# Performance work log

Measured on AMD Instinct MI355X. Metric: run time of the kernel, lower is better.

Reference implementation:

```python
import jax, jax.numpy as jnp
import numpy as np

B, H, W = 2, 512, 512


def _conv(x, w, b):
    y = jax.lax.conv_general_dilated(
        x, w, window_strides=(1, 1), padding='SAME',
        dimension_numbers=('NCHW', 'OIHW', 'NCHW'))
    return y + b[None, :, None, None]


def _pool(x):
    return jax.lax.reduce_window(x, -jnp.inf, jax.lax.max,
                                 (1, 1, 2, 2), (1, 1, 2, 2), 'VALID')


def _vgg_pools(x, ws, bs):
    # vgg16.features up to modules 4, 9, 16 (the first three maxpools)
    r = jax.nn.relu
    x = r(_conv(x, ws[0], bs[0]))
    x = r(_conv(x, ws[1], bs[1]))
    p1 = _pool(x)                      # [B,64,256,256]  (module 4)
    x = r(_conv(p1, ws[2], bs[2]))
    x = r(_conv(x, ws[3], bs[3]))
    p2 = _pool(x)                      # [B,128,128,128] (module 9)
    x = r(_conv(p2, ws[4], bs[4]))
    x = r(_conv(x, ws[5], bs[5]))
    x = r(_conv(x, ws[6], bs[6]))
    p3 = _pool(x)                      # [B,256,64,64]   (module 16)
    return (p1, p2, p3)


def _style(a, g):
    # faithful to per-(b,c) torch.mm(phi.T, phi): WxW Gram per channel
    Bc, C, Hc, Wc = a.shape
    Kp = 1.0 / (C * Hc * Wc)
    Ga = jnp.einsum('bchw,bchv->bcwv', a, a)
    Gg = jnp.einsum('bchw,bchv->bcwv', g, g)
    return jnp.sum(jnp.abs(Kp * (Ga - Gg))) / (C * C)


def setup_inputs() -> dict:
    key = jax.random.key(0)
    ks = jax.random.split(key, 20)
    igt = jax.random.normal(ks[0], (B, 3, H, W), dtype=jnp.float32)
    iout = jax.random.normal(ks[1], (B, 3, H, W), dtype=jnp.float32)
    mask = jax.random.randint(ks[2], (B, 1, H, W), 0, 2).astype(jnp.float32)
    # VGG16 conv stack up to features[16]: channel plan per torchvision vgg16
    chans = [(3, 64), (64, 64), (64, 128), (128, 128), (128, 256), (256, 256), (256, 256)]
    inp = {'igt': igt, 'iout': iout, 'mask': mask}
    for i, (cin, cout) in enumerate(chans):
        scale = np.sqrt(2.0 / (cin * 9)).astype(np.float32)
        inp[f'w{i}'] = jax.random.normal(ks[3 + i], (cout, cin, 3, 3), dtype=jnp.float32) * scale
        inp[f'b{i}'] = jnp.zeros((cout,), dtype=jnp.float32)
    return inp


def reference(igt, iout, mask, w0, b0, w1, b1, w2, b2, w3, b3, w4, b4, w5, b5, w6, b6):
    ws = (w0, w1, w2, w3, w4, w5, w6)
    bs = (b0, b1, b2, b3, b4, b5, b6)
    m = jnp.where(mask != 0, 1.0, 0.0).astype(igt.dtype)   # mask[mask!=0]=1
    icomp = jnp.where(m == 1, igt, iout)                   # make_comp (broadcast over C)
    Bn = igt.shape[0]
    N = 3 * H * W * Bn
    diff = iout - igt
    # l_hole: original loops B times over the FULL norm -> factor B (faithful)
    l_hole = Bn * jnp.sum(jnp.abs((1.0 - m) * diff)) / N
    # l_valid: per-sample norms summed == full L1
    l_valid = jnp.sum(jnp.abs(m * diff)) / N
    pool_out = _vgg_pools(iout, ws, bs)
    pool_gt = _vgg_pools(igt, ws, bs)
    pool_comp = _vgg_pools(icomp, ws, bs)
    # l_perc: original always normalizes by prod(pool_gt[0].shape) (faithful bug)
    Nigt = float(np.prod(pool_gt[0].shape))
    l_perc = 0.0
    for i in range(3):
        l_perc = l_perc + (jnp.sum(jnp.abs(pool_out[i] - pool_gt[i]))
                           + jnp.sum(jnp.abs(pool_comp[i] - pool_gt[i]))) / Nigt
    l_style_comp = sum(_style(pool_comp[i], pool_gt[i]) for i in range(3))
    l_style_out = sum(_style(pool_out[i], pool_gt[i]) for i in range(3))
    return l_hole + l_valid + l_perc + l_style_comp + l_style_out
```

## Files before the change

kernel.cpp:

```cpp
#include <hip/hip_runtime.h>
#include <hip/hip_bf16.h>


typedef __attribute__((ext_vector_type(8))) short bf16x8_t;
typedef __attribute__((ext_vector_type(4))) float f32x4_t;
typedef __attribute__((ext_vector_type(16))) float f32x16_t;
typedef __attribute__((ext_vector_type(8))) int i32x8_t;

typedef const __attribute__((address_space(1))) void* gas_t;
typedef __attribute__((address_space(3))) void* las_t;

__device__ __forceinline__ void gld16(const void* g, void* l) {
  __builtin_amdgcn_global_load_lds((gas_t)g, (las_t)l, 16, 0, 0);
}

__device__ __forceinline__ unsigned char f2fp8(float v) {
  return (unsigned char)(__builtin_amdgcn_cvt_pk_fp8_f32(v, v, 0, false) & 0xff);
}

__device__ __forceinline__ i32x8_t ld_frag(const unsigned char* lds, int row,
                                           int h) {
  const int sw = (row >> 1) & 3;
  const unsigned char* base = lds + row * 64;
  uint4 lo = *(const uint4*)(base + (((2 * h) ^ sw) << 4));
  uint4 hi = *(const uint4*)(base + (((2 * h + 1) ^ sw) << 4));
  i32x8_t r;
  r[0] = lo.x; r[1] = lo.y; r[2] = lo.z; r[3] = lo.w;
  r[4] = hi.x; r[5] = hi.y; r[6] = hi.z; r[7] = hi.w;
  return r;
}

__device__ __forceinline__ i32x8_t ld32g(const unsigned char* p) {
  uint4 lo = *(const uint4*)p;
  uint4 hi = *(const uint4*)(p + 16);
  i32x8_t r;
  r[0] = lo.x; r[1] = lo.y; r[2] = lo.z; r[3] = lo.w;
  r[4] = hi.x; r[5] = hi.y; r[6] = hi.z; r[7] = hi.w;
  return r;
}

__device__ __forceinline__ float blk_sum256(float v, float* s4) {
#pragma unroll
  for (int o = 32; o > 0; o >>= 1) v += __shfl_down(v, o);
  int w = threadIdx.x >> 6;
  if ((threadIdx.x & 63) == 0) s4[w] = v;
  __syncthreads();
  float r = s4[0] + s4[1] + s4[2] + s4[3];
  __syncthreads();
  return r;
}

__global__ void init_slots(float* slots) {
  if (threadIdx.x < 32) slots[threadIdx.x] = 0.0f;
}

__global__ __launch_bounds__(256) void l1_kernel(
    const float* __restrict__ igt, const float* __restrict__ iout,
    const float* __restrict__ mask, float* __restrict__ slots) {
  __shared__ float s4[4];
  float ah = 0.0f, av = 0.0f;
  for (int idx = blockIdx.x * 256 + threadIdx.x; idx < 1572864;
       idx += gridDim.x * 256) {
    int pix = idx & 262143;
    int n = idx / 786432;
    float mk = mask[n * 262144 + pix];
    bool m = (mk != 0.0f);
    float d = fabsf(iout[idx] - igt[idx]);
    if (m) av += d; else ah += d;
  }
  float r = blk_sum256(ah, s4);
  if (threadIdx.x == 0) atomicAdd(&slots[0], r);
  r = blk_sum256(av, s4);
  if (threadIdx.x == 0) atomicAdd(&slots[1], r);
}

__global__ __launch_bounds__(256) void pack_w(const float* __restrict__ w,
                                              unsigned char* __restrict__ wp,
                                              int Cin, int Cout) {
  int i = blockIdx.x * 256 + threadIdx.x;
  int c4n = Cin >> 2;
  if (i >= Cout * c4n * 9) return;
  int o = i % 9;
  int rem = i / 9;
  int c4 = rem % c4n;
  int co = rem / c4n;
  int dy = o / 3, dx = o % 3;
  unsigned r = 0;
#pragma unroll
  for (int k = 0; k < 4; ++k) {
    int ci = c4 * 4 + k;
    float v = w[((co * Cin + ci) * 3 + dy) * 3 + dx];
    r |= (unsigned)f2fp8(v) << (8 * k);
  }
  *(unsigned*)(wp + ((long)(o * Cout + co)) * Cin + c4 * 4) = r;
}

__global__ __launch_bounds__(256) void pack_w1(const float* __restrict__ w,
                                               __hip_bfloat16* __restrict__ wk) {
  int i = blockIdx.x * 256 + threadIdx.x;
  if (i >= 64 * 32) return;
  int co = i >> 5, k = i & 31;
  float v = 0.0f;
  if (k < 27) {
    int dy = k / 9, r = k - dy * 9;
    int dx = r / 3, ci = r - dx * 3;
    v = w[((co * 3 + ci) * 3 + dy) * 3 + dx];
  }
  wk[i] = __float2bfloat16(v);
}

__global__ __launch_bounds__(256) void pack2_kernel(
    const float* __restrict__ igt, const float* __restrict__ iout,
    const float* __restrict__ mask, __hip_bfloat16* __restrict__ apk, int sid,
    int n0, int NB) {
  int idx = blockIdx.x * 256 + threadIdx.x;
  if (idx >= NB * 262144) return;
  int nl = idx >> 18;
  int pix = idx & 262143;
  int y = pix >> 9, x = pix & 511;
  int sample = n0 + nl;
  __align__(16) __hip_bfloat16 buf[32];
#pragma unroll
  for (int k = 27; k < 32; ++k) buf[k] = __float2bfloat16(0.0f);
  for (int dy = 0; dy < 3; ++dy)
    for (int dx = 0; dx < 3; ++dx) {
      int gy = y - 1 + dy, gx = x - 1 + dx;
      bool inb = (gy >= 0 && gy < 512 && gx >= 0 && gx < 512);
      int p = gy * 512 + gx;
      bool useG;
      if (sid == 0) useG = true;
      else if (sid == 1) useG = false;
      else useG = inb && (mask[sample * 262144 + (inb ? p : 0)] != 0.0f);
      const float* src = useG ? igt : iout;
#pragma unroll
      for (int ci = 0; ci < 3; ++ci) {
        float v = inb ? src[sample * 786432 + ci * 262144 + p] : 0.0f;
        buf[dy * 9 + dx * 3 + ci] = __float2bfloat16(v);
      }
    }
  __hip_bfloat16* dst = apk + (long)idx * 32;
#pragma unroll
  for (int q = 0; q < 4; ++q)
    *(uint4*)&dst[q * 8] = *(const uint4*)&buf[q * 8];
}

__global__ __launch_bounds__(256, 2) void conv1m(
    const __hip_bfloat16* __restrict__ apk, const __hip_bfloat16* __restrict__ wk,
    const float* __restrict__ bias, unsigned char* __restrict__ out) {
  __shared__ __align__(16) short ApS[512 * 32];
  __shared__ __align__(16) short BwS[64 * 32];
  const int tid = threadIdx.x;
  const int lane = tid & 63;
  const int wv = tid >> 6;
  const int quad = lane >> 4, l15 = lane & 15;
  const int n = blockIdx.z;
  const int x0 = blockIdx.x << 6;
  const int y0 = blockIdx.y << 3;
  const int spos = lane >> 2;
  const int sq = lane & 3;

  for (int u = wv; u < 32; u += 4) {
    int pos = (u << 4) + spos;
    int r = pos >> 6, c = pos & 63;
    gld16(apk + (((long)n * 512 + y0 + r) * 512 + x0 + c) * 32 + sq * 8,
          &ApS[u << 9]);
  }
  if (wv < 4) gld16(wk + spos * 32 + sq * 8, &BwS[wv << 9]);
  __syncthreads();

  f32x4_t acc[8][4];
#pragma unroll
  for (int mt = 0; mt < 8; ++mt)
#pragma unroll
    for (int nt = 0; nt < 4; ++nt) acc[mt][nt] = (f32x4_t)0.0f;

  bf16x8_t bf[4];
#pragma unroll
  for (int nt = 0; nt < 4; ++nt)
    bf[nt] = *(const bf16x8_t*)&BwS[(nt * 16 + l15) * 32 + quad * 8];
#pragma unroll
  for (int mt = 0; mt < 8; ++mt) {
    const int rl = 2 * wv + (mt >> 2);
    const int pl = (mt & 3) * 16 + l15;
    const bf16x8_t a = *(const bf16x8_t*)&ApS[(rl * 64 + pl) * 32 + quad * 8];
#pragma unroll
    for (int nt = 0; nt < 4; ++nt)
      acc[mt][nt] = __builtin_amdgcn_mfma_f32_16x16x32_bf16(a, bf[nt],
                                                            acc[mt][nt], 0, 0, 0);
  }

  float bv[4];
#pragma unroll
  for (int nt = 0; nt < 4; ++nt) bv[nt] = bias[nt * 16 + l15];

  __syncthreads();
  unsigned char* O8 = (unsigned char*)ApS;
#pragma unroll
  for (int mt = 0; mt < 8; ++mt) {
    const int ry = 2 * wv + (mt >> 2);
#pragma unroll
    for (int nt = 0; nt < 4; ++nt) {
      const int col = nt * 16 + l15;
#pragma unroll
      for (int reg = 0; reg < 4; ++reg) {
        int px = (mt & 3) * 16 + quad * 4 + reg;
        float v = fmaxf(acc[mt][nt][reg] + bv[nt], 0.0f);
        O8[((ry << 6) + px) * 64 + col] = f2fp8(v);
      }
    }
  }
  __syncthreads();
#pragma unroll
  for (int j = 0; j < 8; ++j) {
    int L = (j * 256 + tid) << 4;
    int x = (L >> 6) & 63;
    int cq = L & 63;
    *(uint4*)(out + (((long)n * 512 + y0 + j) * 512 + x0 + x) * 64 + cq) =
        *(const uint4*)&O8[L];
  }
}

__global__ __launch_bounds__(256, 3) void conv_f8(
    const unsigned char* __restrict__ act, const unsigned char* __restrict__ wp,
    const float* __restrict__ bias, unsigned char* __restrict__ out,
    const unsigned char* __restrict__ zp, int Cin, int Cout, int H, int W) {
  __shared__ __align__(16) unsigned char ApS[400 * 64];
  const int tid = threadIdx.x;
  const int lane = tid & 63;
  const int wv = tid >> 6;
  const int l31 = lane & 31;
  const int h = lane >> 5;
  const int pr = wv & 1;
  const int ch = wv >> 1;
  const int coB = Cout >> 6;
  const int n = blockIdx.z / coB;
  const int co0 = (blockIdx.z % coB) << 6;
  const int x0 = blockIdx.x << 6;
  const int y0 = blockIdx.y << 2;
  const int spos = lane >> 2;
  const int sc = lane & 3;

  f32x16_t acc[2][2];
#pragma unroll
  for (int dr = 0; dr < 2; ++dr)
#pragma unroll
    for (int mh = 0; mh < 2; ++mh) acc[dr][mh] = (f32x16_t)0.0f;

  for (int cb = 0; cb < Cin; cb += 64) {
    if (cb) __syncthreads();
    for (int u = wv; u < 25; u += 4) {
      int pos = (u << 4) + spos;
      int q = sc ^ ((pos >> 1) & 3);
      int r = pos / 66, c = pos - r * 66;
      int gy = y0 - 1 + r, gx = x0 - 1 + c;
      const unsigned char* src = zp;
      if (pos < 396 && gy >= 0 && gy < H && gx >= 0 && gx < W)
        src = act + ((long)((long)n * H + gy) * W + gx) * Cin + cb + (q << 4);
      gld16(src, &ApS[u << 10]);
    }
    __syncthreads();

    const unsigned char* wl =
        wp + ((long)(co0 + (ch << 5) + l31)) * Cin + cb + (h << 5);
#pragma unroll
    for (int dx = 0; dx < 3; ++dx) {
      i32x8_t Af[2][4];
#pragma unroll
      for (int mh = 0; mh < 2; ++mh)
#pragma unroll
        for (int ri = 0; ri < 4; ++ri)
          Af[mh][ri] =
              ld_frag(ApS, (2 * pr + ri) * 66 + mh * 32 + l31 + dx, h);
#pragma unroll
      for (int dy = 0; dy < 3; ++dy) {
        const int o = dy * 3 + dx;
        i32x8_t Bf = ld32g(wl + (long)o * Cout * Cin);
#pragma unroll
        for (int dr = 0; dr < 2; ++dr)
#pragma unroll
          for (int mh = 0; mh < 2; ++mh)
            acc[dr][mh] = __builtin_amdgcn_mfma_scale_f32_32x32x64_f8f6f4(
                Af[mh][dr + dy], Bf, acc[dr][mh], 0, 0, 0,
                0x7F7F7F7F, 0, 0x7F7F7F7F);
      }
    }
  }

  const float bv = bias[co0 + (ch << 5) + l31];

  __syncthreads();
#pragma unroll
  for (int dr = 0; dr < 2; ++dr) {
    const int ry = 2 * pr + dr;
#pragma unroll
    for (int mh = 0; mh < 2; ++mh) {
#pragma unroll
      for (int reg = 0; reg < 16; ++reg) {
        int rowM = (reg & 3) + 8 * (reg >> 2) + 4 * h;
        int x = mh * 32 + rowM;
        float v = fmaxf(acc[dr][mh][reg] + bv, 0.0f);
        ApS[((ry << 6) + x) * 64 + (ch << 5) + l31] = f2fp8(v);
      }
    }
  }
  __syncthreads();
#pragma unroll
  for (int j = 0; j < 4; ++j) {
    int L = (j * 256 + tid) << 4;
    int ry = L >> 12;
    int x = (L >> 6) & 63;
    int cq = L & 63;
    *(uint4*)(out + (((long)n * H + y0 + ry) * W + x0 + x) * Cout + co0 + cq) =
        *(const uint4*)&ApS[L];
  }
}

__global__ __launch_bounds__(256, 3) void conv_f8p(
    const unsigned char* __restrict__ act, const unsigned char* __restrict__ wp,
    const float* __restrict__ bias, unsigned char* __restrict__ outF,
    __hip_bfloat16* __restrict__ outB, const unsigned char* __restrict__ zp,
    int Cin, int Cout, int H, int W) {
  __shared__ __align__(16) unsigned char ApS[400 * 64];
  const int tid = threadIdx.x;
  const int lane = tid & 63;
  const int wv = tid >> 6;
  const int l31 = lane & 31;
  const int h = lane >> 5;
  const int pr = wv & 1;
  const int ch = wv >> 1;
  const int coB = Cout >> 6;
  const int n = blockIdx.z / coB;
  const int co0 = (blockIdx.z % coB) << 6;
  const int x0g = blockIdx.x << 6;
  const int y0 = blockIdx.y << 2;
  const int spos = lane >> 2;
  const int sc = lane & 3;

  f32x16_t acc[2][2];
#pragma unroll
  for (int dr = 0; dr < 2; ++dr)
#pragma unroll
    for (int mh = 0; mh < 2; ++mh) acc[dr][mh] = (f32x16_t)0.0f;

  for (int cb = 0; cb < Cin; cb += 64) {
    if (cb) __syncthreads();
    for (int u = wv; u < 25; u += 4) {
      int pos = (u << 4) + spos;
      int q = sc ^ ((pos >> 1) & 3);
      int r = pos / 66, c = pos - r * 66;
      int gy = y0 - 1 + r, gx = x0g - 1 + c;
      const unsigned char* src = zp;
      if (pos < 396 && gy >= 0 && gy < H && gx >= 0 && gx < W)
        src = act + ((long)((long)n * H + gy) * W + gx) * Cin + cb + (q << 4);
      gld16(src, &ApS[u << 10]);
    }
    __syncthreads();

    const unsigned char* wl =
        wp + ((long)(co0 + (ch << 5) + l31)) * Cin + cb + (h << 5);
#pragma unroll
    for (int dx = 0; dx < 3; ++dx) {
      i32x8_t Af[2][4];
#pragma unroll
      for (int mh = 0; mh < 2; ++mh)
#pragma unroll
        for (int ri = 0; ri < 4; ++ri)
          Af[mh][ri] =
              ld_frag(ApS, (2 * pr + ri) * 66 + mh * 32 + l31 + dx, h);
#pragma unroll
      for (int dy = 0; dy < 3; ++dy) {
        const int o = dy * 3 + dx;
        i32x8_t Bf = ld32g(wl + (long)o * Cout * Cin);
#pragma unroll
        for (int dr = 0; dr < 2; ++dr)
#pragma unroll
          for (int mh = 0; mh < 2; ++mh)
            acc[dr][mh] = __builtin_amdgcn_mfma_scale_f32_32x32x64_f8f6f4(
                Af[mh][dr + dy], Bf, acc[dr][mh], 0, 0, 0,
                0x7F7F7F7F, 0, 0x7F7F7F7F);
      }
    }
  }

  const int Ho = H >> 1, Wo = W >> 1;
  const int ho0 = blockIdx.y << 1;
  const int wo0 = blockIdx.x << 5;
  const float bv = bias[co0 + (ch << 5) + l31];

  __syncthreads();
  unsigned char* F8 = ApS;
  __hip_bfloat16* BB = (__hip_bfloat16*)(ApS + 4096);
#pragma unroll
  for (int mh = 0; mh < 2; ++mh) {
#pragma unroll
    for (int p8 = 0; p8 < 8; ++p8) {
      const int reg = 2 * p8;
      float m0 = fmaxf(fmaxf(acc[0][mh][reg], acc[0][mh][reg + 1]),
                       fmaxf(acc[1][mh][reg], acc[1][mh][reg + 1]));
      float v = fmaxf(m0 + bv, 0.0f);
      int rowM = (reg & 3) + 8 * (reg >> 2) + 4 * h;
      int wo = mh * 16 + (rowM >> 1);
      int off = ((pr * 32 + wo) << 6) + (ch << 5) + l31;
      F8[off] = f2fp8(v);
      BB[off] = __float2bfloat16(v);
    }
  }
  __syncthreads();
  {
    int L = tid << 4;
    int hl = L >> 11;
    int wo = (L >> 6) & 31;
    int cq = L & 63;
    *(uint4*)(outF + (((long)n * Ho + ho0 + hl) * Wo + wo0 + wo) * Cout + co0 +
              cq) = *(const uint4*)&F8[L];
  }
#pragma unroll
  for (int j = 0; j < 2; ++j) {
    int S = (j * 256 + tid) << 3;
    int hl = S >> 11;
    int wo = (S >> 6) & 31;
    int cq = S & 63;
    *(uint4*)(outB + (((long)n * Ho + ho0 + hl) * Wo + wo0 + wo) * Cout + co0 +
              cq) = *(const uint4*)&BB[S];
  }
}

__global__ __launch_bounds__(256) void transpose_k(
    const __hip_bfloat16* __restrict__ in, __hip_bfloat16* __restrict__ out,
    int C, int Ho, int Wo) {
  const int cl = threadIdx.x & 31;
  const int wl = threadIdx.x >> 5;
  const int cg = C >> 5;
  const int j = blockIdx.z / cg;
  const int c = (blockIdx.z % cg) * 32 + cl;
  const int wo = blockIdx.x * 8 + wl;
  const int ho0 = blockIdx.y * 8;
  __align__(16) __hip_bfloat16 res[8];
#pragma unroll
  for (int i = 0; i < 8; ++i)
    res[i] = in[(((long)j * Ho + ho0 + i) * Wo + wo) * C + c];
  *(uint4*)&out[((long)(j * C + c) * Wo + wo) * Ho + ho0] =
      *(const uint4*)res;
}

__global__ __launch_bounds__(256) void perc_kernel(
    const __hip_bfloat16* __restrict__ gt, const __hip_bfloat16* __restrict__ cur,
    int M8, float* __restrict__ slots) {
  __shared__ float s4[4];
  const uint4* g4 = (const uint4*)gt;
  const uint4* c4 = (const uint4*)cur;
  float acc = 0.0f;
  for (int i = blockIdx.x * 256 + threadIdx.x; i < M8; i += gridDim.x * 256) {
    uint4 g = g4[i], c = c4[i];
    const unsigned* gu = (const unsigned*)&g;
    const unsigned* cu = (const unsigned*)&c;
#pragma unroll
    for (int k = 0; k < 4; ++k) {
      float g0 = __uint_as_float(gu[k] << 16);
      float g1 = __uint_as_float(gu[k] & 0xffff0000u);
      float c0 = __uint_as_float(cu[k] << 16);
      float c1 = __uint_as_float(cu[k] & 0xffff0000u);
      acc += fabsf(c0 - g0) + fabsf(c1 - g1);
    }
  }
  float r = blk_sum256(acc, s4);
  if (threadIdx.x == 0) atomicAdd(&slots[2], r);
}

template <int BM>
__global__ __launch_bounds__(256) void gram_mfma(
    const __hip_bfloat16* __restrict__ gt_p,
    const __hip_bfloat16* __restrict__ cur_p, int Wp, int Hp, float fscale,
    float* __restrict__ slots) {
  constexpr int COLS = BM + 64;
  constexpr int WR = BM / 4;
  constexpr int MT = WR / 16;
  __shared__ __align__(16) short S[2 * COLS * 40];
  __shared__ float s4[4];
  const int tid = threadIdx.x;
  const int lane = tid & 63;
  const int wvi = tid >> 6;
  const int quad = lane >> 4, l15 = lane & 15;
  const int vt = blockIdx.x * 64;
  const int wt = blockIdx.y * BM;
  const long plane = (long)blockIdx.z * Wp * Hp;
  const __hip_bfloat16* bases[2] = {gt_p + plane, cur_p + plane};

  f32x4_t acc[2][MT][4];
#pragma unroll
  for (int t = 0; t < 2; ++t)
#pragma unroll
    for (int mt = 0; mt < MT; ++mt)
#pragma unroll
      for (int nt = 0; nt < 4; ++nt) acc[t][mt][nt] = (f32x4_t)0.0f;

  const int nchunk = 2 * COLS * 4;
  for (int h0 = 0; h0 < Hp; h0 += 32) {
    for (int e = tid; e < nchunk; e += 256) {
      int chunk = e & 3;
      int colt = e >> 2;
      int t = colt / COLS;
      int col = colt - t * COLS;
      int sc = (col < BM) ? (wt + col) : (vt + col - BM);
      uint4 v = *(const uint4*)(bases[t] + (long)sc * Hp + h0 + chunk * 8);
      *(uint4*)&S[(t * COLS + col) * 40 + chunk * 8] = v;
    }
    __syncthreads();
#pragma unroll
    for (int t = 0; t < 2; ++t) {
      bf16x8_t bf[4];
#pragma unroll
      for (int nt = 0; nt < 4; ++nt)
        bf[nt] = *(const bf16x8_t*)&S[(t * COLS + BM + nt * 16 + l15) * 40 +
                                      quad * 8];
#pragma unroll
      for (int mt = 0; mt < MT; ++mt) {
        bf16x8_t a = *(const bf16x8_t*)&S[(t * COLS + wvi * WR + mt * 16 + l15) *
                                              40 + quad * 8];
#pragma unroll
        for (int nt = 0; nt < 4; ++nt)
          acc[t][mt][nt] = __builtin_amdgcn_mfma_f32_16x16x32_bf16(
              a, bf[nt], acc[t][mt][nt], 0, 0, 0);
      }
    }
    __syncthreads();
  }

  float local = 0.0f;
#pragma unroll
  for (int mt = 0; mt < MT; ++mt)
#pragma unroll
    for (int nt = 0; nt < 4; ++nt)
#pragma unroll
      for (int reg = 0; reg < 4; ++reg)
        local += fabsf(acc[1][mt][nt][reg] - acc[0][mt][nt][reg]);
  float r = blk_sum256(local, s4);
  if (tid == 0) atomicAdd(&slots[3], r * fscale);
}

__global__ void combine_kernel(const float* __restrict__ slots,
                               float* __restrict__ out) {
  if (threadIdx.x == 0) {
    const float Nn = 1572864.0f;
    const float Nigt = 8388608.0f;
    out[0] = 2.0f * slots[0] / Nn + slots[1] / Nn + slots[2] / Nigt + slots[3];
  }
}

extern "C" void kernel_launch(void* const* d_in, const int* in_sizes, int n_in,
                              void* d_out, int out_size, void* d_ws,
                              size_t ws_size, hipStream_t stream) {
  (void)in_sizes; (void)n_in; (void)out_size;
  const float* igt = (const float*)d_in[0];
  const float* iout = (const float*)d_in[1];
  const float* mask = (const float*)d_in[2];
  const float* w[7];
  const float* b[7];
  for (int i = 0; i < 7; ++i) {
    w[i] = (const float*)d_in[3 + 2 * i];
    b[i] = (const float*)d_in[4 + 2 * i];
  }
  float* slots = (float*)d_ws;
  const unsigned char* zp = (const unsigned char*)d_ws + 64;

  unsigned char* wpk = (unsigned char*)((char*)d_ws + 256);
  const long wpOff[6] = {0, 36864, 110592, 258048, 552960, 1142784};
  const int wpCin[6] = {64, 64, 128, 128, 256, 256};
  const int wpCout[6] = {64, 128, 128, 256, 256, 256};
  __hip_bfloat16* w1k = (__hip_bfloat16*)((char*)d_ws + 256 + 1732608);

  const size_t NEED2 = 194674944ULL;
  const int NB = (ws_size >= NEED2) ? 2 : 1;
  const int B3 = 3 * NB;

  char* base = (char*)d_ws + 1736960;
  __hip_bfloat16* Apk = (__hip_bfloat16*)base;
  unsigned char* Y1 = (unsigned char*)(base + (size_t)NB * 16777216);
  unsigned char* P1N8 = (unsigned char*)(base + (size_t)NB * 33554432);
  __hip_bfloat16* P1Nb = (__hip_bfloat16*)(base + (size_t)NB * 46137344);
  __hip_bfloat16* pgT1 = (__hip_bfloat16*)(base + (size_t)NB * 54525952);
  __hip_bfloat16* pcT1 = (__hip_bfloat16*)(base + (size_t)NB * 62914560);
  __hip_bfloat16* P2Nb = (__hip_bfloat16*)(base + (size_t)NB * 71303168);
  __hip_bfloat16* P2T = (__hip_bfloat16*)(base + (size_t)NB * 83886080);
  unsigned char* T = (unsigned char*)base;
  unsigned char* P2N8 = (unsigned char*)(base + (size_t)NB * 46137344);
  unsigned char* Y5 = (unsigned char*)base;
  unsigned char* Y6 = (unsigned char*)(base + (size_t)NB * 12582912);
  __hip_bfloat16* P3Nb = (__hip_bfloat16*)(base + (size_t)NB * 33554432);
  __hip_bfloat16* P3T = (__hip_bfloat16*)(base + (size_t)NB * 39845888);
  unsigned char* P3N8 = (unsigned char*)(base + (size_t)NB * 46137344);

  const float fs1 = (float)(1.0 / (4194304.0 * 4096.0));
  const float fs2 = (float)(1.0 / (2097152.0 * 16384.0));
  const float fs3 = (float)(1.0 / (1048576.0 * 65536.0));

  init_slots<<<1, 64, 0, stream>>>(slots);
  l1_kernel<<<304, 256, 0, stream>>>(igt, iout, mask, slots);
  for (int l = 0; l < 6; ++l) {
    int elems = wpCout[l] * (wpCin[l] >> 2) * 9;
    pack_w<<<(elems + 255) / 256, 256, 0, stream>>>(w[l + 1], wpk + wpOff[l],
                                                    wpCin[l], wpCout[l]);
  }
  pack_w1<<<8, 256, 0, stream>>>(w[0], w1k);

  for (int n0 = 0; n0 < 2; n0 += NB) {
    for (int s = 0; s < 3; ++s) {
      pack2_kernel<<<NB * 1024, 256, 0, stream>>>(igt, iout, mask, Apk, s, n0, NB);
      conv1m<<<dim3(8, 64, NB), 256, 0, stream>>>(Apk, w1k, b[0], Y1);
      conv_f8p<<<dim3(8, 128, NB), 256, 0, stream>>>(
          Y1, wpk + wpOff[0], b[1], P1N8 + (size_t)s * NB * 4194304, P1Nb, zp,
          64, 64, 512, 512);
      transpose_k<<<dim3(32, 32, NB * 2), 256, 0, stream>>>(
          P1Nb, (s ? pcT1 : pgT1), 64, 256, 256);
      if (s > 0) {
        perc_kernel<<<304, 256, 0, stream>>>(pgT1, pcT1, NB * 524288, slots);
        gram_mfma<128><<<dim3(4, 2, NB * 64), 256, 0, stream>>>(
            pgT1, pcT1, 256, 256, fs1, slots);
      }
    }
    conv_f8<<<dim3(4, 64, B3 * 2), 256, 0, stream>>>(
        P1N8, wpk + wpOff[1], b[2], T, zp, 64, 128, 256, 256);
    conv_f8p<<<dim3(4, 64, B3 * 2), 256, 0, stream>>>(
        T, wpk + wpOff[2], b[3], P2N8, P2Nb, zp, 128, 128, 256, 256);
    transpose_k<<<dim3(16, 16, B3 * 4), 256, 0, stream>>>(P2Nb, P2T, 128, 128, 128);
    for (int s = 1; s <= 2; ++s) {
      perc_kernel<<<304, 256, 0, stream>>>(
          P2T, P2T + (size_t)s * NB * 2097152, NB * 262144, slots);
      gram_mfma<128><<<dim3(2, 1, NB * 128), 256, 0, stream>>>(
          P2T, P2T + (size_t)s * NB * 2097152, 128, 128, fs2, slots);
    }
    conv_f8<<<dim3(2, 32, B3 * 4), 256, 0, stream>>>(
        P2N8, wpk + wpOff[3], b[4], Y5, zp, 128, 256, 128, 128);
    conv_f8<<<dim3(2, 32, B3 * 4), 256, 0, stream>>>(
        Y5, wpk + wpOff[4], b[5], Y6, zp, 256, 256, 128, 128);
    conv_f8p<<<dim3(2, 32, B3 * 4), 256, 0, stream>>>(
        Y6, wpk + wpOff[5], b[6], P3N8, P3Nb, zp, 256, 256, 128, 128);
    transpose_k<<<dim3(8, 8, B3 * 8), 256, 0, stream>>>(P3Nb, P3T, 256, 64, 64);
    for (int s = 1; s <= 2; ++s) {
      perc_kernel<<<304, 256, 0, stream>>>(
          P3T, P3T + (size_t)s * NB * 1048576, NB * 131072, slots);
      gram_mfma<64><<<dim3(1, 1, NB * 256), 256, 0, stream>>>(
          P3T, P3T + (size_t)s * NB * 1048576, 64, 64, fs3, slots);
    }
  }

  combine_kernel<<<1, 64, 0, stream>>>(slots, (float*)d_out);
}
```

Measured before the change: 828.4 us.

## Double-buffer LDS staging in fp8 convs and process two row tiles per block

```diff
diff --git a/kernel.cpp b/kernel.cpp
--- a/kernel.cpp
+++ b/kernel.cpp
@@ -220,11 +220,11 @@
   }
 }
 
-__global__ __launch_bounds__(256, 3) void conv_f8(
+__global__ __launch_bounds__(256, 2) void conv_f8(
     const unsigned char* __restrict__ act, const unsigned char* __restrict__ wp,
     const float* __restrict__ bias, unsigned char* __restrict__ out,
     const unsigned char* __restrict__ zp, int Cin, int Cout, int H, int W) {
-  __shared__ __align__(16) unsigned char ApS[400 * 64];
+  __shared__ __align__(16) unsigned char ApS[2][28 * 1024];
   const int tid = threadIdx.x;
   const int lane = tid & 63;
   const int wv = tid >> 6;
@@ -236,32 +236,60 @@
   const int n = blockIdx.z / coB;
   const int co0 = (blockIdx.z % coB) << 6;
   const int x0 = blockIdx.x << 6;
-  const int y0 = blockIdx.y << 2;
+  const int y0base = blockIdx.y << 3;
   const int spos = lane >> 2;
   const int sc = lane & 3;
-
-  f32x16_t acc[2][2];
-#pragma unroll
-  for (int dr = 0; dr < 2; ++dr)
-#pragma unroll
-    for (int mh = 0; mh < 2; ++mh) acc[dr][mh] = (f32x16_t)0.0f;
-
-  for (int cb = 0; cb < Cin; cb += 64) {
-    if (cb) __syncthreads();
-    for (int u = wv; u < 25; u += 4) {
-      int pos = (u << 4) + spos;
+  const int CB = Cin >> 6;
+  const int NU = 2 * CB;
+  const float bv = bias[co0 + (ch << 5) + l31];
+
+  auto STAGE = [&](int u) {
+    const int t = u / CB;
+    const int cb64 = (u - t * CB) << 6;
+    const int ty0 = y0base + t * 4;
+    unsigned char* dst = ApS[u & 1];
+    for (int uu = wv; uu < 28; uu += 4) {
+      int pos = (uu << 4) + spos;
       int q = sc ^ ((pos >> 1) & 3);
       int r = pos / 66, c = pos - r * 66;
-      int gy = y0 - 1 + r, gx = x0 - 1 + c;
+      int gy = ty0 - 1 + r, gx = x0 - 1 + c;
       const unsigned char* src = zp;
       if (pos < 396 && gy >= 0 && gy < H && gx >= 0 && gx < W)
-        src = act + ((long)((long)n * H + gy) * W + gx) * Cin + cb + (q << 4);
-      gld16(src, &ApS[u << 10]);
-    }
-    __syncthreads();
+        src = act + ((long)((long)n * H + gy) * W + gx) * Cin + cb64 + (q << 4);
+      gld16(src, dst + (uu << 10));
+    }
+  };
+
+  f32x16_t acc[2][2];
+#pragma unroll
+  for (int dr = 0; dr < 2; ++dr)
+#pragma unroll
+    for (int mh = 0; mh < 2; ++mh) acc[dr][mh] = (f32x16_t)0.0f;
+
+  STAGE(0);
+  for (int u = 0; u < NU; ++u) {
+    const int t = u / CB;
+    const int cb = u - t * CB;
+    const int ty0 = y0base + t * 4;
+    if (u == 0) {
+      asm volatile("s_waitcnt vmcnt(0)" ::: "memory");
+    } else if (cb == 0) {
+      asm volatile("s_waitcnt vmcnt(4)" ::: "memory");
+    } else {
+      asm volatile("s_waitcnt vmcnt(0)" ::: "memory");
+    }
+    __builtin_amdgcn_s_barrier();
 
     const unsigned char* wl =
-        wp + ((long)(co0 + (ch << 5) + l31)) * Cin + cb + (h << 5);
+        wp + ((long)(co0 + (ch << 5) + l31)) * Cin + (cb << 6) + (h << 5);
+    i32x8_t Bh[9];
+#pragma unroll
+    for (int o = 0; o < 9; ++o) Bh[o] = ld32g(wl + (long)o * Cout * Cin);
+    __builtin_amdgcn_sched_barrier(0);
+    if (u + 1 < NU) STAGE(u + 1);
+    __builtin_amdgcn_sched_barrier(0);
+
+    const unsigned char* A = ApS[u & 1];
 #pragma unroll
     for (int dx = 0; dx < 3; ++dx) {
       i32x8_t Af[2][4];
@@ -269,58 +297,61 @@
       for (int mh = 0; mh < 2; ++mh)
 #pragma unroll
         for (int ri = 0; ri < 4; ++ri)
-          Af[mh][ri] =
-              ld_frag(ApS, (2 * pr + ri) * 66 + mh * 32 + l31 + dx, h);
+          Af[mh][ri] = ld_frag(A, (2 * pr + ri) * 66 + mh * 32 + l31 + dx, h);
 #pragma unroll
       for (int dy = 0; dy < 3; ++dy) {
-        const int o = dy * 3 + dx;
-        i32x8_t Bf = ld32g(wl + (long)o * Cout * Cin);
 #pragma unroll
         for (int dr = 0; dr < 2; ++dr)
 #pragma unroll
           for (int mh = 0; mh < 2; ++mh)
             acc[dr][mh] = __builtin_amdgcn_mfma_scale_f32_32x32x64_f8f6f4(
-                Af[mh][dr + dy], Bf, acc[dr][mh], 0, 0, 0,
+                Af[mh][dr + dy], Bh[dy * 3 + dx], acc[dr][mh], 0, 0, 0,
                 0x7F7F7F7F, 0, 0x7F7F7F7F);
       }
     }
-  }
-
-  const float bv = bias[co0 + (ch << 5) + l31];
-
-  __syncthreads();
-#pragma unroll
-  for (int dr = 0; dr < 2; ++dr) {
-    const int ry = 2 * pr + dr;
-#pragma unroll
-    for (int mh = 0; mh < 2; ++mh) {
-#pragma unroll
-      for (int reg = 0; reg < 16; ++reg) {
-        int rowM = (reg & 3) + 8 * (reg >> 2) + 4 * h;
-        int x = mh * 32 + rowM;
-        float v = fmaxf(acc[dr][mh][reg] + bv, 0.0f);
-        ApS[((ry << 6) + x) * 64 + (ch << 5) + l31] = f2fp8(v);
-      }
-    }
-  }
-  __syncthreads();
-#pragma unroll
-  for (int j = 0; j < 4; ++j) {
-    int L = (j * 256 + tid) << 4;
-    int ry = L >> 12;
-    int x = (L >> 6) & 63;
-    int cq = L & 63;
-    *(uint4*)(out + (((long)n * H + y0 + ry) * W + x0 + x) * Cout + co0 + cq) =
-        *(const uint4*)&ApS[L];
-  }
-}
-
-__global__ __launch_bounds__(256, 3) void conv_f8p(
+
+    if (cb == CB - 1) {
+      unsigned char* O8 = ApS[u & 1];
+      __builtin_amdgcn_s_barrier();
+#pragma unroll
+      for (int dr = 0; dr < 2; ++dr) {
+        const int ry = 2 * pr + dr;
+#pragma unroll
+        for (int mh = 0; mh < 2; ++mh) {
+#pragma unroll
+          for (int reg = 0; reg < 16; ++reg) {
+            int rowM = (reg & 3) + 8 * (reg >> 2) + 4 * h;
+            int x = mh * 32 + rowM;
+            float v = fmaxf(acc[dr][mh][reg] + bv, 0.0f);
+            O8[((ry << 6) + x) * 64 + (ch << 5) + l31] = f2fp8(v);
+          }
+        }
+      }
+      asm volatile("s_waitcnt lgkmcnt(0)" ::: "memory");
+      __builtin_amdgcn_s_barrier();
+#pragma unroll
+      for (int j = 0; j < 4; ++j) {
+        int L = (j * 256 + tid) << 4;
+        int ry = L >> 12;
+        int x = (L >> 6) & 63;
+        int cq = L & 63;
+        *(uint4*)(out + (((long)n * H + ty0 + ry) * W + x0 + x) * Cout + co0 +
+                  cq) = *(const uint4*)&O8[L];
+      }
+#pragma unroll
+      for (int dr = 0; dr < 2; ++dr)
+#pragma unroll
+        for (int mh = 0; mh < 2; ++mh) acc[dr][mh] = (f32x16_t)0.0f;
+    }
+  }
+}
+
+__global__ __launch_bounds__(256, 2) void conv_f8p(
     const unsigned char* __restrict__ act, const unsigned char* __restrict__ wp,
     const float* __restrict__ bias, unsigned char* __restrict__ outF,
     __hip_bfloat16* __restrict__ outB, const unsigned char* __restrict__ zp,
     int Cin, int Cout, int H, int W) {
-  __shared__ __align__(16) unsigned char ApS[400 * 64];
+  __shared__ __align__(16) unsigned char ApS[2][28 * 1024];
   const int tid = threadIdx.x;
   const int lane = tid & 63;
   const int wv = tid >> 6;
@@ -331,33 +362,63 @@
   const int coB = Cout >> 6;
   const int n = blockIdx.z / coB;
   const int co0 = (blockIdx.z % coB) << 6;
-  const int x0g = blockIdx.x << 6;
-  const int y0 = blockIdx.y << 2;
+  const int x0 = blockIdx.x << 6;
+  const int y0base = blockIdx.y << 3;
   const int spos = lane >> 2;
   const int sc = lane & 3;
-
-  f32x16_t acc[2][2];
-#pragma unroll
-  for (int dr = 0; dr < 2; ++dr)
-#pragma unroll
-    for (int mh = 0; mh < 2; ++mh) acc[dr][mh] = (f32x16_t)0.0f;
-
-  for (int cb = 0; cb < Cin; cb += 64) {
-    if (cb) __syncthreads();
-    for (int u = wv; u < 25; u += 4) {
-      int pos = (u << 4) + spos;
+  const int CB = Cin >> 6;
+  const int NU = 2 * CB;
+  const int Ho = H >> 1, Wo = W >> 1;
+  const int wo0 = blockIdx.x << 5;
+  const float bv = bias[co0 + (ch << 5) + l31];
+
+  auto STAGE = [&](int u) {
+    const int t = u / CB;
+    const int cb64 = (u - t * CB) << 6;
+    const int ty0 = y0base + t * 4;
+    unsigned char* dst = ApS[u & 1];
+    for (int uu = wv; uu < 28; uu += 4) {
+      int pos = (uu << 4) + spos;
       int q = sc ^ ((pos >> 1) & 3);
       int r = pos / 66, c = pos - r * 66;
-      int gy = y0 - 1 + r, gx = x0g - 1 + c;
+      int gy = ty0 - 1 + r, gx = x0 - 1 + c;
       const unsigned char* src = zp;
       if (pos < 396 && gy >= 0 && gy < H && gx >= 0 && gx < W)
-        src = act + ((long)((long)n * H + gy) * W + gx) * Cin + cb + (q << 4);
-      gld16(src, &ApS[u << 10]);
-    }
-    __syncthreads();
+        src = act + ((long)((long)n * H + gy) * W + gx) * Cin + cb64 + (q << 4);
+      gld16(src, dst + (uu << 10));
+    }
+  };
+
+  f32x16_t acc[2][2];
+#pragma unroll
+  for (int dr = 0; dr < 2; ++dr)
+#pragma unroll
+    for (int mh = 0; mh < 2; ++mh) acc[dr][mh] = (f32x16_t)0.0f;
+
+  STAGE(0);
+  for (int u = 0; u < NU; ++u) {
+    const int t = u / CB;
+    const int cb = u - t * CB;
+    const int ty0 = y0base + t * 4;
+    if (u == 0) {
+      asm volatile("s_waitcnt vmcnt(0)" ::: "memory");
+    } else if (cb == 0) {
+      asm volatile("s_waitcnt vmcnt(3)" ::: "memory");
+    } else {
+      asm volatile("s_waitcnt vmcnt(0)" ::: "memory");
+    }
+    __builtin_amdgcn_s_barrier();
 
     const unsigned char* wl =
-        wp + ((long)(co0 + (ch << 5) + l31)) * Cin + cb + (h << 5);
+        wp + ((long)(co0 + (ch << 5) + l31)) * Cin + (cb << 6) + (h << 5);
+    i32x8_t Bh[9];
+#pragma unroll
+    for (int o = 0; o < 9; ++o) Bh[o] = ld32g(wl + (long)o * Cout * Cin);
+    __builtin_amdgcn_sched_barrier(0);
+    if (u + 1 < NU) STAGE(u + 1);
+    __builtin_amdgcn_sched_barrier(0);
+
+    const unsigned char* A = ApS[u & 1];
 #pragma unroll
     for (int dx = 0; dx < 3; ++dx) {
       i32x8_t Af[2][4];
@@ -365,63 +426,63 @@
       for (int mh = 0; mh < 2; ++mh)
 #pragma unroll
         for (int ri = 0; ri < 4; ++ri)
-          Af[mh][ri] =
-              ld_frag(ApS, (2 * pr + ri) * 66 + mh * 32 + l31 + dx, h);
+          Af[mh][ri] = ld_frag(A, (2 * pr + ri) * 66 + mh * 32 + l31 + dx, h);
 #pragma unroll
       for (int dy = 0; dy < 3; ++dy) {
-        const int o = dy * 3 + dx;
-        i32x8_t Bf = ld32g(wl + (long)o * Cout * Cin);
 #pragma unroll
         for (int dr = 0; dr < 2; ++dr)
 #pragma unroll
           for (int mh = 0; mh < 2; ++mh)
             acc[dr][mh] = __builtin_amdgcn_mfma_scale_f32_32x32x64_f8f6f4(
-                Af[mh][dr + dy], Bf, acc[dr][mh], 0, 0, 0,
+                Af[mh][dr + dy], Bh[dy * 3 + dx], acc[dr][mh], 0, 0, 0,
                 0x7F7F7F7F, 0, 0x7F7F7F7F);
       }
     }
-  }
-
-  const int Ho = H >> 1, Wo = W >> 1;
-  const int ho0 = blockIdx.y << 1;
-  const int wo0 = blockIdx.x << 5;
-  const float bv = bias[co0 + (ch << 5) + l31];
-
-  __syncthreads();
-  unsigned char* F8 = ApS;
-  __hip_bfloat16* BB = (__hip_bfloat16*)(ApS + 4096);
-#pragma unroll
-  for (int mh = 0; mh < 2; ++mh) {
-#pragma unroll
-    for (int p8 = 0; p8 < 8; ++p8) {
-      const int reg = 2 * p8;
-      float m0 = fmaxf(fmaxf(acc[0][mh][reg], acc[0][mh][reg + 1]),
-                       fmaxf(acc[1][mh][reg], acc[1][mh][reg + 1]));
-      float v = fmaxf(m0 + bv, 0.0f);
-      int rowM = (reg & 3) + 8 * (reg >> 2) + 4 * h;
-      int wo = mh * 16 + (rowM >> 1);
-      int off = ((pr * 32 + wo) << 6) + (ch << 5) + l31;
-      F8[off] = f2fp8(v);
-      BB[off] = __float2bfloat16(v);
-    }
-  }
-  __syncthreads();
-  {
-    int L = tid << 4;
-    int hl = L >> 11;
-    int wo = (L >> 6) & 31;
-    int cq = L & 63;
-    *(uint4*)(outF + (((long)n * Ho + ho0 + hl) * Wo + wo0 + wo) * Cout + co0 +
-              cq) = *(const uint4*)&F8[L];
-  }
-#pragma unroll
-  for (int j = 0; j < 2; ++j) {
-    int S = (j * 256 + tid) << 3;
-    int hl = S >> 11;
-    int wo = (S >> 6) & 31;
-    int cq = S & 63;
-    *(uint4*)(outB + (((long)n * Ho + ho0 + hl) * Wo + wo0 + wo) * Cout + co0 +
-              cq) = *(const uint4*)&BB[S];
+
+    if (cb == CB - 1) {
+      const int ho0 = (ty0 >> 1);
+      unsigned char* F8 = ApS[u & 1];
+      __hip_bfloat16* BB = (__hip_bfloat16*)(ApS[u & 1] + 4096);
+      __builtin_amdgcn_s_barrier();
+#pragma unroll
+      for (int mh = 0; mh < 2; ++mh) {
+#pragma unroll
+        for (int p8 = 0; p8 < 8; ++p8) {
+          const int reg = 2 * p8;
+          float m0 = fmaxf(fmaxf(acc[0][mh][reg], acc[0][mh][reg + 1]),
+                           fmaxf(acc[1][mh][reg], acc[1][mh][reg + 1]));
+          float v = fmaxf(m0 + bv, 0.0f);
+          int rowM = (reg & 3) + 8 * (reg >> 2) + 4 * h;
+          int wo = mh * 16 + (rowM >> 1);
+          int off = ((pr * 32 + wo) << 6) + (ch << 5) + l31;
+          F8[off] = f2fp8(v);
+          BB[off] = __float2bfloat16(v);
+        }
+      }
+      asm volatile("s_waitcnt lgkmcnt(0)" ::: "memory");
+      __builtin_amdgcn_s_barrier();
+      {
+        int L = tid << 4;
+        int hl = L >> 11;
+        int wo = (L >> 6) & 31;
+        int cq = L & 63;
+        *(uint4*)(outF + (((long)n * Ho + ho0 + hl) * Wo + wo0 + wo) * Cout +
+                  co0 + cq) = *(const uint4*)&F8[L];
+      }
+#pragma unroll
+      for (int j = 0; j < 2; ++j) {
+        int S = (j * 256 + tid) << 3;
+        int hl = S >> 11;
+        int wo = (S >> 6) & 31;
+        int cq = S & 63;
+        *(uint4*)(outB + (((long)n * Ho + ho0 + hl) * Wo + wo0 + wo) * Cout +
+                  co0 + cq) = *(const uint4*)&BB[S];
+      }
+#pragma unroll
+      for (int dr = 0; dr < 2; ++dr)
+#pragma unroll
+        for (int mh = 0; mh < 2; ++mh) acc[dr][mh] = (f32x16_t)0.0f;
+    }
   }
 }
 
@@ -607,7 +668,7 @@
     for (int s = 0; s < 3; ++s) {
       pack2_kernel<<<NB * 1024, 256, 0, stream>>>(igt, iout, mask, Apk, s, n0, NB);
       conv1m<<<dim3(8, 64, NB), 256, 0, stream>>>(Apk, w1k, b[0], Y1);
-      conv_f8p<<<dim3(8, 128, NB), 256, 0, stream>>>(
+      conv_f8p<<<dim3(8, 64, NB), 256, 0, stream>>>(
           Y1, wpk + wpOff[0], b[1], P1N8 + (size_t)s * NB * 4194304, P1Nb, zp,
           64, 64, 512, 512);
       transpose_k<<<dim3(32, 32, NB * 2), 256, 0, stream>>>(
@@ -618,9 +679,9 @@
             pgT1, pcT1, 256, 256, fs1, slots);
       }
     }
-    conv_f8<<<dim3(4, 64, B3 * 2), 256, 0, stream>>>(
+    conv_f8<<<dim3(4, 32, B3 * 2), 256, 0, stream>>>(
         P1N8, wpk + wpOff[1], b[2], T, zp, 64, 128, 256, 256);
-    conv_f8p<<<dim3(4, 64, B3 * 2), 256, 0, stream>>>(
+    conv_f8p<<<dim3(4, 32, B3 * 2), 256, 0, stream>>>(
         T, wpk + wpOff[2], b[3], P2N8, P2Nb, zp, 128, 128, 256, 256);
     transpose_k<<<dim3(16, 16, B3 * 4), 256, 0, stream>>>(P2Nb, P2T, 128, 128, 128);
     for (int s = 1; s <= 2; ++s) {
@@ -629,11 +690,11 @@
       gram_mfma<128><<<dim3(2, 1, NB * 128), 256, 0, stream>>>(
           P2T, P2T + (size_t)s * NB * 2097152, 128, 128, fs2, slots);
     }
-    conv_f8<<<dim3(2, 32, B3 * 4), 256, 0, stream>>>(
+    conv_f8<<<dim3(2, 16, B3 * 4), 256, 0, stream>>>(
         P2N8, wpk + wpOff[3], b[4], Y5, zp, 128, 256, 128, 128);
-    conv_f8<<<dim3(2, 32, B3 * 4), 256, 0, stream>>>(
+    conv_f8<<<dim3(2, 16, B3 * 4), 256, 0, stream>>>(
         Y5, wpk + wpOff[4], b[5], Y6, zp, 256, 256, 128, 128);
-    conv_f8p<<<dim3(2, 32, B3 * 4), 256, 0, stream>>>(
+    conv_f8p<<<dim3(2, 16, B3 * 4), 256, 0, stream>>>(
         Y6, wpk + wpOff[5], b[6], P3N8, P3Nb, zp, 256, 256, 128, 128);
     transpose_k<<<dim3(8, 8, B3 * 8), 256, 0, stream>>>(P3Nb, P3T, 256, 64, 64);
     for (int s = 1; s <= 2; ++s) {
```

New measurement: 887.4 us. 7.1% more time.

## Batch all three streams into single launches and drop unused fp8 pool output

Applied to the files above, without the earlier changes.

```diff
diff --git a/kernel.cpp b/kernel.cpp
--- a/kernel.cpp
+++ b/kernel.cpp
@@ -401,12 +401,12 @@
       int rowM = (reg & 3) + 8 * (reg >> 2) + 4 * h;
       int wo = mh * 16 + (rowM >> 1);
       int off = ((pr * 32 + wo) << 6) + (ch << 5) + l31;
-      F8[off] = f2fp8(v);
+      if (outF) F8[off] = f2fp8(v);
       BB[off] = __float2bfloat16(v);
     }
   }
   __syncthreads();
-  {
+  if (outF) {
     int L = tid << 4;
     int hl = L >> 11;
     int wo = (L >> 6) & 31;
@@ -445,13 +445,14 @@
 
 __global__ __launch_bounds__(256) void perc_kernel(
     const __hip_bfloat16* __restrict__ gt, const __hip_bfloat16* __restrict__ cur,
-    int M8, float* __restrict__ slots) {
+    int M8, int gN, float* __restrict__ slots) {
   __shared__ float s4[4];
   const uint4* g4 = (const uint4*)gt;
   const uint4* c4 = (const uint4*)cur;
   float acc = 0.0f;
   for (int i = blockIdx.x * 256 + threadIdx.x; i < M8; i += gridDim.x * 256) {
-    uint4 g = g4[i], c = c4[i];
+    int ig = (i >= gN) ? i - gN : i;
+    uint4 g = g4[ig], c = c4[i];
     const unsigned* gu = (const unsigned*)&g;
     const unsigned* cu = (const unsigned*)&c;
 #pragma unroll
@@ -470,8 +471,8 @@
 template <int BM>
 __global__ __launch_bounds__(256) void gram_mfma(
     const __hip_bfloat16* __restrict__ gt_p,
-    const __hip_bfloat16* __restrict__ cur_p, int Wp, int Hp, float fscale,
-    float* __restrict__ slots) {
+    const __hip_bfloat16* __restrict__ cur_p, int Wp, int Hp, int gtm,
+    float fscale, float* __restrict__ slots) {
   constexpr int COLS = BM + 64;
   constexpr int WR = BM / 4;
   constexpr int MT = WR / 16;
@@ -484,7 +485,8 @@
   const int vt = blockIdx.x * 64;
   const int wt = blockIdx.y * BM;
   const long plane = (long)blockIdx.z * Wp * Hp;
-  const __hip_bfloat16* bases[2] = {gt_p + plane, cur_p + plane};
+  const long plane_g = (long)(blockIdx.z % gtm) * Wp * Hp;
+  const __hip_bfloat16* bases[2] = {gt_p + plane_g, cur_p + plane};
 
   f32x4_t acc[2][MT][4];
 #pragma unroll
@@ -572,23 +574,25 @@
   const size_t NEED2 = 194674944ULL;
   const int NB = (ws_size >= NEED2) ? 2 : 1;
   const int B3 = 3 * NB;
+  const size_t M = (size_t)NB;
 
   char* base = (char*)d_ws + 1736960;
   __hip_bfloat16* Apk = (__hip_bfloat16*)base;
-  unsigned char* Y1 = (unsigned char*)(base + (size_t)NB * 16777216);
-  unsigned char* P1N8 = (unsigned char*)(base + (size_t)NB * 33554432);
-  __hip_bfloat16* P1Nb = (__hip_bfloat16*)(base + (size_t)NB * 46137344);
-  __hip_bfloat16* pgT1 = (__hip_bfloat16*)(base + (size_t)NB * 54525952);
-  __hip_bfloat16* pcT1 = (__hip_bfloat16*)(base + (size_t)NB * 62914560);
-  __hip_bfloat16* P2Nb = (__hip_bfloat16*)(base + (size_t)NB * 71303168);
-  __hip_bfloat16* P2T = (__hip_bfloat16*)(base + (size_t)NB * 83886080);
-  unsigned char* T = (unsigned char*)base;
-  unsigned char* P2N8 = (unsigned char*)(base + (size_t)NB * 46137344);
-  unsigned char* Y5 = (unsigned char*)base;
-  unsigned char* Y6 = (unsigned char*)(base + (size_t)NB * 12582912);
-  __hip_bfloat16* P3Nb = (__hip_bfloat16*)(base + (size_t)NB * 33554432);
-  __hip_bfloat16* P3T = (__hip_bfloat16*)(base + (size_t)NB * 39845888);
-  unsigned char* P3N8 = (unsigned char*)(base + (size_t)NB * 46137344);
+  unsigned char* P1N8 = (unsigned char*)base;
+  __hip_bfloat16* P2T = (__hip_bfloat16*)base;
+  char* Y1base = base + M * 16777216;
+  unsigned char* Y1 = (unsigned char*)Y1base;
+  __hip_bfloat16* pgT1 = (__hip_bfloat16*)Y1base;
+  __hip_bfloat16* pcT1 = (__hip_bfloat16*)(Y1base + M * 8388608);
+  unsigned char* P2N8 = (unsigned char*)(Y1base + M * 25165824);
+  __hip_bfloat16* P2Nb = (__hip_bfloat16*)(Y1base + M * 31457280);
+  __hip_bfloat16* P3Nb = (__hip_bfloat16*)Y1base;
+  __hip_bfloat16* P3T = (__hip_bfloat16*)(Y1base + M * 6291456);
+  char* Cbase = base + M * 67108864;
+  __hip_bfloat16* P1Nb = (__hip_bfloat16*)Cbase;
+  unsigned char* T = (unsigned char*)Cbase;
+  unsigned char* Y5 = (unsigned char*)Cbase;
+  unsigned char* Y6 = (unsigned char*)(Cbase + M * 12582912);
 
   const float fs1 = (float)(1.0 / (4194304.0 * 4096.0));
   const float fs2 = (float)(1.0 / (2097152.0 * 16384.0));
@@ -605,43 +609,43 @@
 
   for (int n0 = 0; n0 < 2; n0 += NB) {
     for (int s = 0; s < 3; ++s) {
-      pack2_kernel<<<NB * 1024, 256, 0, stream>>>(igt, iout, mask, Apk, s, n0, NB);
-      conv1m<<<dim3(8, 64, NB), 256, 0, stream>>>(Apk, w1k, b[0], Y1);
-      conv_f8p<<<dim3(8, 128, NB), 256, 0, stream>>>(
-          Y1, wpk + wpOff[0], b[1], P1N8 + (size_t)s * NB * 4194304, P1Nb, zp,
-          64, 64, 512, 512);
-      transpose_k<<<dim3(32, 32, NB * 2), 256, 0, stream>>>(
-          P1Nb, (s ? pcT1 : pgT1), 64, 256, 256);
-      if (s > 0) {
-        perc_kernel<<<304, 256, 0, stream>>>(pgT1, pcT1, NB * 524288, slots);
-        gram_mfma<128><<<dim3(4, 2, NB * 64), 256, 0, stream>>>(
-            pgT1, pcT1, 256, 256, fs1, slots);
-      }
-    }
+      pack2_kernel<<<NB * 1024, 256, 0, stream>>>(igt, iout, mask, Apk, s, n0,
+                                                  NB);
+      conv1m<<<dim3(8, 64, NB), 256, 0, stream>>>(
+          Apk, w1k, b[0], Y1 + (size_t)s * M * 16777216);
+    }
+    conv_f8p<<<dim3(8, 128, 3 * NB), 256, 0, stream>>>(
+        Y1, wpk + wpOff[0], b[1], P1N8, P1Nb, zp, 64, 64, 512, 512);
+    transpose_k<<<dim3(32, 32, 3 * NB * 2), 256, 0, stream>>>(P1Nb, pgT1, 64,
+                                                              256, 256);
+    perc_kernel<<<304, 256, 0, stream>>>(pgT1, pcT1, NB * 1048576,
+                                         NB * 524288, slots);
+    gram_mfma<128><<<dim3(4, 2, NB * 128), 256, 0, stream>>>(
+        pgT1, pcT1, 256, 256, NB * 64, fs1, slots);
+
     conv_f8<<<dim3(4, 64, B3 * 2), 256, 0, stream>>>(
         P1N8, wpk + wpOff[1], b[2], T, zp, 64, 128, 256, 256);
     conv_f8p<<<dim3(4, 64, B3 * 2), 256, 0, stream>>>(
         T, wpk + wpOff[2], b[3], P2N8, P2Nb, zp, 128, 128, 256, 256);
-    transpose_k<<<dim3(16, 16, B3 * 4), 256, 0, stream>>>(P2Nb, P2T, 128, 128, 128);
-    for (int s = 1; s <= 2; ++s) {
-      perc_kernel<<<304, 256, 0, stream>>>(
-          P2T, P2T + (size_t)s * NB * 2097152, NB * 262144, slots);
-      gram_mfma<128><<<dim3(2, 1, NB * 128), 256, 0, stream>>>(
-          P2T, P2T + (size_t)s * NB * 2097152, 128, 128, fs2, slots);
-    }
+    transpose_k<<<dim3(16, 16, B3 * 4), 256, 0, stream>>>(P2Nb, P2T, 128, 128,
+                                                          128);
+    perc_kernel<<<304, 256, 0, stream>>>(P2T, P2T + M * 2097152, NB * 524288,
+                                         NB * 262144, slots);
+    gram_mfma<128><<<dim3(2, 1, NB * 256), 256, 0, stream>>>(
+        P2T, P2T + M * 2097152, 128, 128, NB * 128, fs2, slots);
+
     conv_f8<<<dim3(2, 32, B3 * 4), 256, 0, stream>>>(
         P2N8, wpk + wpOff[3], b[4], Y5, zp, 128, 256, 128, 128);
     conv_f8<<<dim3(2, 32, B3 * 4), 256, 0, stream>>>(
         Y5, wpk + wpOff[4], b[5], Y6, zp, 256, 256, 128, 128);
     conv_f8p<<<dim3(2, 32, B3 * 4), 256, 0, stream>>>(
-        Y6, wpk + wpOff[5], b[6], P3N8, P3Nb, zp, 256, 256, 128, 128);
+        Y6, wpk + wpOff[5], b[6], (unsigned char*)nullptr, P3Nb, zp, 256, 256,
+        128, 128);
     transpose_k<<<dim3(8, 8, B3 * 8), 256, 0, stream>>>(P3Nb, P3T, 256, 64, 64);
-    for (int s = 1; s <= 2; ++s) {
-      perc_kernel<<<304, 256, 0, stream>>>(
-          P3T, P3T + (size_t)s * NB * 1048576, NB * 131072, slots);
-      gram_mfma<64><<<dim3(1, 1, NB * 256), 256, 0, stream>>>(
-          P3T, P3T + (size_t)s * NB * 1048576, 64, 64, fs3, slots);
-    }
+    perc_kernel<<<304, 256, 0, stream>>>(P3T, P3T + M * 1048576, NB * 262144,
+                                         NB * 131072, slots);
+    gram_mfma<64><<<dim3(1, 1, NB * 512), 256, 0, stream>>>(
+        P3T, P3T + M * 1048576, 64, 64, NB * 256, fs3, slots);
   }
 
   combine_kernel<<<1, 64, 0, stream>>>(slots, (float*)d_out);
```

New measurement: 769.0 us. 7.2% less time.
